# Kernel optimization log

Measured on AMD Instinct MI355X. Metric: run time of the kernel, lower is better.

The kernel has to match this reference:

```python
import jax, jax.numpy as jnp
import numpy as np

V, E, H, L = 32000, 512, 512, 2   # vocab, emb_dim, hidden_dim, lstm layers
IN = 2 * H                        # input_size (= enc_output feature dim)
B, S_ENC, T_DEC = 32, 128, 64


def setup_inputs() -> dict:
    key = jax.random.key(0)
    ks = jax.random.split(key, 20)
    sc = 0.05
    inp = {
        "tokens": jax.random.randint(ks[0], (B, T_DEC), 0, V),
        "enc_output": jax.random.normal(ks[1], (B, S_ENC, IN), jnp.float32),
        "enc_h": jax.random.normal(ks[2], (L, B, H), jnp.float32),
        "enc_c": jax.random.normal(ks[3], (L, B, H), jnp.float32),
        "emb": jax.random.normal(ks[4], (V, E), jnp.float32) * sc,
        # attention MLP: attn1 in = H*L + IN, out = 4H; attn2: 4H -> 1
        "attn1_w": jax.random.normal(ks[5], (4 * H, H * L + IN), jnp.float32) * sc,
        "attn1_b": jnp.zeros((4 * H,), jnp.float32),
        "attn2_w": jax.random.normal(ks[6], (1, 4 * H), jnp.float32) * sc,
        "attn2_b": jnp.zeros((1,), jnp.float32),
        # LSTM layer 0: input E + IN; layer 1: input H. PyTorch gate order i,f,g,o
        "w_ih0": jax.random.normal(ks[7], (4 * H, E + IN), jnp.float32) * sc,
        "w_hh0": jax.random.normal(ks[8], (4 * H, H), jnp.float32) * sc,
        "b_ih0": jnp.zeros((4 * H,), jnp.float32),
        "b_hh0": jnp.zeros((4 * H,), jnp.float32),
        "w_ih1": jax.random.normal(ks[9], (4 * H, H), jnp.float32) * sc,
        "w_hh1": jax.random.normal(ks[10], (4 * H, H), jnp.float32) * sc,
        "b_ih1": jnp.zeros((4 * H,), jnp.float32),
        "b_hh1": jnp.zeros((4 * H,), jnp.float32),
        "out_w": jax.random.normal(ks[11], (V, H), jnp.float32) * sc,
        "out_b": jnp.zeros((V,), jnp.float32),
    }
    return inp


def _lstm_cell(x, h, c, w_ih, w_hh, b_ih, b_hh):
    g = x @ w_ih.T + h @ w_hh.T + (b_ih + b_hh)
    i, f, gg, o = jnp.split(g, 4, axis=-1)
    c_new = jax.nn.sigmoid(f) * c + jax.nn.sigmoid(i) * jnp.tanh(gg)
    h_new = jax.nn.sigmoid(o) * jnp.tanh(c_new)
    return h_new, c_new


def reference(tokens, enc_output, enc_h, enc_c, emb,
              attn1_w, attn1_b, attn2_w, attn2_b,
              w_ih0, w_hh0, b_ih0, b_hh0,
              w_ih1, w_hh1, b_ih1, b_hh1,
              out_w, out_b):
    b, s_enc = enc_output.shape[0], enc_output.shape[1]

    def context(h):  # h: [L, B, H] -> context: [B, 2H]
        hflat = jnp.transpose(h, (1, 0, 2)).reshape(b, -1)          # [B, L*H]
        hexp = jnp.broadcast_to(hflat[:, None, :], (b, s_enc, hflat.shape[-1]))
        ai = jnp.concatenate([enc_output, hexp], axis=-1)           # [B, S, 2H+L*H]
        hid = ai @ attn1_w.T + attn1_b                               # [B, S, 4H]
        logits = hid @ attn2_w.T + attn2_b                           # [B, S, 1]
        w = jax.nn.softmax(logits, axis=1)
        return jnp.sum(enc_output * w, axis=1)                       # [B, 2H]

    def step(carry, emb_t):  # emb_t: [B, E]
        h, c = carry
        ctx = context(h)
        x = jnp.concatenate([emb_t, ctx], axis=-1)                   # [B, E+2H]
        h0, c0 = _lstm_cell(x, h[0], c[0], w_ih0, w_hh0, b_ih0, b_hh0)
        h1, c1 = _lstm_cell(h0, h[1], c[1], w_ih1, w_hh1, b_ih1, b_hh1)
        return (jnp.stack([h0, h1]), jnp.stack([c0, c1])), h1

    emb_seq = jnp.transpose(emb[tokens], (1, 0, 2))                  # [T, B, E]
    _, outs = jax.lax.scan(step, (enc_h, enc_c), emb_seq)            # [T, B, H]
    dec = jnp.transpose(outs, (1, 0, 2))                             # [B, T, H]
    return dec @ out_w.T + out_b                                     # [B, T, V]
```

## Files before the change

### kernel.cpp

```cpp
#include <hip/hip_runtime.h>
#include <hip/hip_bf16.h>

typedef __attribute__((ext_vector_type(4))) float f4v;
typedef __attribute__((ext_vector_type(4))) short s4v;
typedef __attribute__((ext_vector_type(8))) short s8v;

#define DEVINL __device__ __forceinline__
#define NBLK 128
#define PADK 536
#define WROWS (16 * PADK)
#define HSLOT 16384

DEVINL short f2bf(float f) {
  unsigned u = __float_as_uint(f);
  u += 0x7FFFu + ((u >> 16) & 1u);
  return (short)(u >> 16);
}
DEVINL float bf2f(short s) {
  return __uint_as_float(((unsigned)(unsigned short)s) << 16);
}
DEVINL float sigm(float x) { return 1.f / (1.f + expf(-x)); }

DEVINL void cstore64(short* p, unsigned long long d) {
  asm volatile("global_store_dwordx2 %0, %1, off sc0 sc1"
               :: "v"(p), "v"(d) : "memory");
}

__global__ __launch_bounds__(256) void k_init2(const float* __restrict__ enc_h,
                                               short* __restrict__ hbuf,
                                               unsigned* __restrict__ arr) {
  int i = blockIdx.x * 256 + threadIdx.x;
  hbuf[i] = f2bf(enc_h[i]);
  hbuf[(long)65 * HSLOT + i] = f2bf(enc_h[16384 + i]);
  if (i < NBLK * 32 + 32) arr[i] = 0u;
}

__global__ __launch_bounds__(256) void k_weff(const float* __restrict__ attn1_w,
                                              const float* __restrict__ attn2_w,
                                              float* __restrict__ w_enc) {
  __shared__ float part[8][32];
  int t = threadIdx.x;
  int jl = t & 31, kp = t >> 5;
  int j = blockIdx.x * 32 + jl;
  float acc = 0.f;
  for (int k = kp * 256; k < kp * 256 + 256; ++k)
    acc += attn2_w[k] * attn1_w[(long)k * 2048 + j];
  part[kp][jl] = acc;
  __syncthreads();
  if (t < 32) {
    float s = 0.f;
    for (int p = 0; p < 8; ++p) s += part[p][t];
    w_enc[blockIdx.x * 32 + t] = s;
  }
}

__global__ __launch_bounds__(256) void k_attn(const float* __restrict__ enc,
                                              const float* __restrict__ w_enc,
                                              float* __restrict__ ctx) {
  __shared__ float red[256];
  __shared__ float wls[128];
  int b = blockIdx.x, t = threadIdx.x;
  int s = t >> 1, half = t & 1;
  const float* e = enc + ((long)b * 128 + s) * 1024 + half * 512;
  const float* wv = w_enc + half * 512;
  float acc = 0.f;
  for (int k = 0; k < 512; k += 4) {
    f4v ev = *(const f4v*)(e + k);
    f4v w4 = *(const f4v*)(wv + k);
    acc += ev[0] * w4[0] + ev[1] * w4[1] + ev[2] * w4[2] + ev[3] * w4[3];
  }
  red[t] = acc;
  __syncthreads();
  if (half == 0) wls[s] = red[t] + red[t + 1];
  __syncthreads();
  red[t] = (t < 128) ? wls[t] : -3.4e38f;
  __syncthreads();
  for (int off = 128; off >= 1; off >>= 1) {
    if (t < off) red[t] = fmaxf(red[t], red[t + off]);
    __syncthreads();
  }
  float mx = red[0];
  __syncthreads();
  if (t < 128) { float ex = expf(wls[t] - mx); wls[t] = ex; red[t] = ex; }
  else red[t] = 0.f;
  __syncthreads();
  for (int off = 128; off >= 1; off >>= 1) {
    if (t < off) red[t] += red[t + off];
    __syncthreads();
  }
  float inv = 1.f / red[0];
  __syncthreads();
  if (t < 128) wls[t] *= inv;
  __syncthreads();
  float a0 = 0.f, a1 = 0.f, a2 = 0.f, a3 = 0.f;
  for (int ss = 0; ss < 128; ++ss) {
    float w = wls[ss];
    const float* er = enc + ((long)b * 128 + ss) * 1024;
    a0 += w * er[t];
    a1 += w * er[t + 256];
    a2 += w * er[t + 512];
    a3 += w * er[t + 768];
  }
  ctx[b * 1024 + t] = a0;
  ctx[b * 1024 + t + 256] = a1;
  ctx[b * 1024 + t + 512] = a2;
  ctx[b * 1024 + t + 768] = a3;
}

__global__ __launch_bounds__(256) void k_ctxpre(const float* __restrict__ w_ih0,
                                                const float* __restrict__ b_ih0,
                                                const float* __restrict__ b_hh0,
                                                const float* __restrict__ ctx,
                                                float* __restrict__ ctxpre) {
  int t = threadIdx.x;
  int j = blockIdx.x * 8 + (t >> 5);
  int b = t & 31;
  float acc = b_ih0[j] + b_hh0[j];
  const float* w = w_ih0 + (long)j * 1536 + 512;
  const float* c = ctx + b * 1024;
  for (int k = 0; k < 1024; k += 4) {
    f4v wv = *(const f4v*)(w + k);
    f4v cv = *(const f4v*)(c + k);
    acc += wv[0] * cv[0] + wv[1] * cv[1] + wv[2] * cv[2] + wv[3] * cv[3];
  }
  ctxpre[b * 2048 + j] = acc;
}

__global__ __launch_bounds__(256) void k_cvt(const float* __restrict__ src,
                                             short* __restrict__ dst) {
  long i = ((long)blockIdx.x * 256 + threadIdx.x) * 8;
  f4v a = *(const f4v*)(src + i);
  f4v b = *(const f4v*)(src + i + 4);
  s8v o;
  o[0] = f2bf(a[0]); o[1] = f2bf(a[1]); o[2] = f2bf(a[2]); o[3] = f2bf(a[3]);
  o[4] = f2bf(b[0]); o[5] = f2bf(b[1]); o[6] = f2bf(b[2]); o[7] = f2bf(b[3]);
  *(s8v*)(dst + i) = o;
}

template <int MODE>
__global__ __launch_bounds__(256) void gemm_bf16(
    const float* __restrict__ A, const float* __restrict__ B,
    const int* __restrict__ a_rows, const float* __restrict__ bias,
    float* __restrict__ C, int K, int lda, int ldb, int ldc) {
  __shared__ short As[128 * 72];
  __shared__ short Bs[128 * 72];
  int n0 = blockIdx.x * 128, m0 = blockIdx.y * 128;
  int t = threadIdx.x;
  int lane = t & 63, w = t >> 6;
  int wm = w & 1, wn = w >> 1;
  f4v acc[4][4];
#pragma unroll
  for (int mi = 0; mi < 4; ++mi)
#pragma unroll
    for (int ni = 0; ni < 4; ++ni) acc[mi][ni] = (f4v){0.f, 0.f, 0.f, 0.f};

  int sr = t >> 1;
  int sh = (t & 1) * 32;
  long arow = a_rows ? (long)a_rows[m0 + sr] : (long)(m0 + sr);
  const float* ap = A + arow * lda + sh;
  const float* bp = B + (long)(n0 + sr) * ldb + sh;
  short* as = &As[sr * 72 + sh];
  short* bs = &Bs[sr * 72 + sh];

  for (int k0 = 0; k0 < K; k0 += 64) {
#pragma unroll
    for (int i = 0; i < 8; ++i) {
      f4v va = *(const f4v*)(ap + k0 + i * 4);
      f4v vb = *(const f4v*)(bp + k0 + i * 4);
      s4v sa, sb;
      sa[0] = f2bf(va[0]); sa[1] = f2bf(va[1]); sa[2] = f2bf(va[2]); sa[3] = f2bf(va[3]);
      sb[0] = f2bf(vb[0]); sb[1] = f2bf(vb[1]); sb[2] = f2bf(vb[2]); sb[3] = f2bf(vb[3]);
      *(s4v*)(as + i * 4) = sa;
      *(s4v*)(bs + i * 4) = sb;
    }
    __syncthreads();
#pragma unroll
    for (int ks = 0; ks < 2; ++ks) {
      s8v af[4], bf[4];
#pragma unroll
      for (int mi = 0; mi < 4; ++mi)
        af[mi] = *(const s8v*)&As[(wm * 64 + mi * 16 + (lane & 15)) * 72 + ks * 32 + (lane >> 4) * 8];
#pragma unroll
      for (int ni = 0; ni < 4; ++ni)
        bf[ni] = *(const s8v*)&Bs[(wn * 64 + ni * 16 + (lane & 15)) * 72 + ks * 32 + (lane >> 4) * 8];
#pragma unroll
      for (int mi = 0; mi < 4; ++mi)
#pragma unroll
        for (int ni = 0; ni < 4; ++ni)
          acc[mi][ni] = __builtin_amdgcn_mfma_f32_16x16x32_bf16(af[mi], bf[ni], acc[mi][ni], 0, 0, 0);
    }
    __syncthreads();
  }
  int fq = lane >> 4, fr = lane & 15;
#pragma unroll
  for (int mi = 0; mi < 4; ++mi)
#pragma unroll
    for (int ni = 0; ni < 4; ++ni) {
      int col = n0 + wn * 64 + ni * 16 + fr;
      long rowb = m0 + wm * 64 + mi * 16 + fq * 4;
      if (MODE == 2) {
        int bz = (col & 511) >> 2;
        int c = ((col >> 9) << 2) + (col & 3);
#pragma unroll
        for (int r = 0; r < 4; ++r) {
          long m = rowb + r;
          C[(long)bz * 32768 + (m & 63) * 512 + (m >> 6) * 16 + c] = acc[mi][ni][r];
        }
      } else {
        float bv = bias ? bias[col] : 0.f;
#pragma unroll
        for (int r = 0; r < 4; ++r) C[(rowb + r) * (long)ldc + col] = acc[mi][ni][r] + bv;
      }
    }
}

template <bool BCVT>
__global__ __launch_bounds__(256) void gemm_out(
    const short* __restrict__ A, const short* __restrict__ Bbf,
    const float* __restrict__ Bf, const float* __restrict__ bias,
    float* __restrict__ C) {
  __shared__ short As[128 * 72];
  __shared__ short Bs[128 * 72];
  int m0 = blockIdx.x * 128, n0 = blockIdx.y * 128;
  int t = threadIdx.x;
  int lane = t & 63, w = t >> 6;
  int wm = w & 1, wn = w >> 1;
  f4v acc[4][4];
#pragma unroll
  for (int mi = 0; mi < 4; ++mi)
#pragma unroll
    for (int ni = 0; ni < 4; ++ni) acc[mi][ni] = (f4v){0.f, 0.f, 0.f, 0.f};

  int sr = t >> 1;
  int sh = (t & 1) * 32;
  const short* ap = A + (long)(m0 + sr) * 512 + sh;
  const short* bpb = Bbf + (long)(n0 + sr) * 512 + sh;
  const float* bpf = Bf + (long)(n0 + sr) * 512 + sh;
  short* as = &As[sr * 72 + sh];
  short* bs = &Bs[sr * 72 + sh];

  for (int k0 = 0; k0 < 512; k0 += 64) {
#pragma unroll
    for (int i = 0; i < 4; ++i)
      *(s8v*)(as + i * 8) = *(const s8v*)(ap + k0 + i * 8);
    if (BCVT) {
#pragma unroll
      for (int i = 0; i < 8; ++i) {
        f4v vb = *(const f4v*)(bpf + k0 + i * 4);
        s4v sb;
        sb[0] = f2bf(vb[0]); sb[1] = f2bf(vb[1]); sb[2] = f2bf(vb[2]); sb[3] = f2bf(vb[3]);
        *(s4v*)(bs + i * 4) = sb;
      }
    } else {
#pragma unroll
      for (int i = 0; i < 4; ++i)
        *(s8v*)(bs + i * 8) = *(const s8v*)(bpb + k0 + i * 8);
    }
    __syncthreads();
#pragma unroll
    for (int ks = 0; ks < 2; ++ks) {
      s8v af[4], bf[4];
#pragma unroll
      for (int mi = 0; mi < 4; ++mi)
        af[mi] = *(const s8v*)&As[(wm * 64 + mi * 16 + (lane & 15)) * 72 + ks * 32 + (lane >> 4) * 8];
#pragma unroll
      for (int ni = 0; ni < 4; ++ni)
        bf[ni] = *(const s8v*)&Bs[(wn * 64 + ni * 16 + (lane & 15)) * 72 + ks * 32 + (lane >> 4) * 8];
#pragma unroll
      for (int mi = 0; mi < 4; ++mi)
#pragma unroll
        for (int ni = 0; ni < 4; ++ni)
          acc[mi][ni] = __builtin_amdgcn_mfma_f32_16x16x32_bf16(af[mi], bf[ni], acc[mi][ni], 0, 0, 0);
    }
    __syncthreads();
  }
  int fq = lane >> 4, fr = lane & 15;
#pragma unroll
  for (int mi = 0; mi < 4; ++mi)
#pragma unroll
    for (int ni = 0; ni < 4; ++ni) {
      int col = n0 + wn * 64 + ni * 16 + fr;
      float bv = bias[col];
      long rowb = m0 + wm * 64 + mi * 16 + fq * 4;
#pragma unroll
      for (int r = 0; r < 4; ++r)
        __builtin_nontemporal_store(acc[mi][ni][r] + bv, &C[(rowb + r) * 32000L + col]);
    }
}

__global__ __launch_bounds__(256, 1) void lstm_persist(
    const float* __restrict__ w_hh0, const float* __restrict__ w_ih1,
    const float* __restrict__ w_hh1,
    const float* __restrict__ b_ih1, const float* __restrict__ b_hh1,
    const float* __restrict__ enc_c,
    const float* __restrict__ embp2, const float* __restrict__ ctxpre,
    short* __restrict__ hbuf, short* __restrict__ h1seqbf,
    unsigned* __restrict__ arr) {
  __shared__ alignas(16) short wlds[6 * WROWS];
  __shared__ float ctxp_l[32][16];
  __shared__ float bias1_l[16];
  __shared__ float gbuf[2][2][32][17];

  const int tid = threadIdx.x;
  const int hb4 = blockIdx.x * 4;
  const int lane = tid & 63, wid = tid >> 6;
  const int mt = wid & 1, kh = wid >> 1;
  const int fr = lane & 15, fq = lane >> 4;

  for (int base = tid * 4; base < 48 * 512; base += 1024) {
    int row = base >> 9, k = base & 511;
    int m = row >> 4, c = row & 15;
    int j = ((c >> 2) << 9) + hb4 + (c & 3);
    const float* wsrc = (m == 0) ? w_hh0 : ((m == 1) ? w_ih1 : w_hh1);
    f4v v = *(const f4v*)(wsrc + (long)j * 512 + k);
    short* hi = &wlds[(m * 2) * WROWS + c * PADK + k];
    short* lo = &wlds[(m * 2 + 1) * WROWS + c * PADK + k];
#pragma unroll
    for (int e = 0; e < 4; ++e) {
      short hh = f2bf(v[e]);
      hi[e] = hh;
      lo[e] = f2bf(v[e] - bf2f(hh));
    }
  }
  for (int i = tid; i < 512; i += 256) {
    int b = i >> 4, c = i & 15;
    ctxp_l[b][c] = ctxpre[b * 2048 + ((c >> 2) << 9) + hb4 + (c & 3)];
  }
  if (tid < 16) {
    int j = ((tid >> 2) << 9) + hb4 + (tid & 3);
    bias1_l[tid] = b_ih1[j] + b_hh1[j];
  }
  const int cq = (tid & 127) >> 2, cr = tid & 3;
  float c0r = 0.f, c1r = 0.f;
  if (tid < 128) c0r = enc_c[cq * 512 + hb4 + cr];
  else           c1r = enc_c[16384 + cq * 512 + hb4 + cr];
  __syncthreads();
  asm volatile("s_waitcnt vmcnt(0)" ::: "memory");
  asm volatile("buffer_inv sc1" ::: "memory");
  __syncthreads();

  short* H0 = hbuf;
  short* H1 = hbuf + (long)65 * HSLOT;
  const int foff = (mt * 16 + fr) * 512 + kh * 256 + fq * 8;
  const int woff = fr * PADK + kh * 256 + fq * 8;

  for (int p = 0; p <= 64; ++p) {
    const bool do_l0 = (p < 64), do_l1 = (p > 0);
    if (p) {
      if (tid < NBLK)
        while (__hip_atomic_load(&arr[tid << 5], __ATOMIC_RELAXED,
                                 __HIP_MEMORY_SCOPE_AGENT) < (unsigned)p)
          __builtin_amdgcn_s_sleep(2);
      __syncthreads();
    }
    float e4[4] = {0.f, 0.f, 0.f, 0.f};
    if (do_l0 && tid < 128) {
      const float* ep = embp2 + (long)blockIdx.x * 32768 + p * 512 + cq * 16 + cr;
#pragma unroll
      for (int g = 0; g < 4; ++g) e4[g] = ep[g * 4];
    }
    {
      f4v l0h = {0.f, 0.f, 0.f, 0.f}, l0l = l0h;
      f4v x1h = l0h, x1l = l0h, h1h = l0h, h1l = l0h;
      const short* a0 = H0 + (long)p * HSLOT + foff;
      const short* a1 = H1 + (long)(do_l1 ? p - 1 : 0) * HSLOT + foff;
      const short* b0h = &wlds[0 * WROWS + woff];
      const short* b0l = &wlds[1 * WROWS + woff];
      const short* b2h = &wlds[2 * WROWS + woff];
      const short* b2l = &wlds[3 * WROWS + woff];
      const short* b4h = &wlds[4 * WROWS + woff];
      const short* b4l = &wlds[5 * WROWS + woff];
#pragma unroll
      for (int ks = 0; ks < 8; ++ks) {
        s8v A0 = *(const s8v*)(a0 + ks * 32);
        if (do_l0) {
          s8v B0h = *(const s8v*)(b0h + ks * 32);
          s8v B0l = *(const s8v*)(b0l + ks * 32);
          l0h = __builtin_amdgcn_mfma_f32_16x16x32_bf16(A0, B0h, l0h, 0, 0, 0);
          l0l = __builtin_amdgcn_mfma_f32_16x16x32_bf16(A0, B0l, l0l, 0, 0, 0);
        }
        if (do_l1) {
          s8v B2h = *(const s8v*)(b2h + ks * 32);
          s8v B2l = *(const s8v*)(b2l + ks * 32);
          x1h = __builtin_amdgcn_mfma_f32_16x16x32_bf16(A0, B2h, x1h, 0, 0, 0);
          x1l = __builtin_amdgcn_mfma_f32_16x16x32_bf16(A0, B2l, x1l, 0, 0, 0);
          s8v A1 = *(const s8v*)(a1 + ks * 32);
          s8v B4h = *(const s8v*)(b4h + ks * 32);
          s8v B4l = *(const s8v*)(b4l + ks * 32);
          h1h = __builtin_amdgcn_mfma_f32_16x16x32_bf16(A1, B4h, h1h, 0, 0, 0);
          h1l = __builtin_amdgcn_mfma_f32_16x16x32_bf16(A1, B4l, h1l, 0, 0, 0);
        }
      }
      if (do_l0) {
        f4v s = l0h + l0l;
#pragma unroll
        for (int r = 0; r < 4; ++r) gbuf[0][kh][mt * 16 + fq * 4 + r][fr] = s[r];
      }
      if (do_l1) {
        f4v s = x1h + x1l + h1h + h1l;
#pragma unroll
        for (int r = 0; r < 4; ++r) gbuf[1][kh][mt * 16 + fq * 4 + r][fr] = s[r];
      }
    }
    __syncthreads();
    if (tid < 128) {
      if (do_l0) {
        float g4[4];
#pragma unroll
        for (int g = 0; g < 4; ++g) {
          int c = g * 4 + cr;
          g4[g] = gbuf[0][0][cq][c] + gbuf[0][1][cq][c] + ctxp_l[cq][c] + e4[g];
        }
        float cn = sigm(g4[1]) * c0r + sigm(g4[0]) * tanhf(g4[2]);
        float hn = sigm(g4[3]) * tanhf(cn);
        c0r = cn;
        unsigned v16 = (unsigned)(unsigned short)f2bf(hn);
        unsigned p01 = v16 | ((unsigned)__shfl_down((int)v16, 1) << 16);
        unsigned long long wd = (unsigned long long)p01 |
            ((unsigned long long)(unsigned)__shfl_down((int)p01, 2) << 32);
        if ((tid & 3) == 0)
          cstore64(H0 + (long)(p + 1) * HSLOT + cq * 512 + hb4, wd);
      }
    } else if (do_l1) {
      float g4[4];
#pragma unroll
      for (int g = 0; g < 4; ++g) {
        int c = g * 4 + cr;
        g4[g] = gbuf[1][0][cq][c] + gbuf[1][1][cq][c] + bias1_l[c];
      }
      float cn = sigm(g4[1]) * c1r + sigm(g4[0]) * tanhf(g4[2]);
      float hn = sigm(g4[3]) * tanhf(cn);
      c1r = cn;
      unsigned v16 = (unsigned)(unsigned short)f2bf(hn);
      unsigned p01 = v16 | ((unsigned)__shfl_down((int)v16, 1) << 16);
      unsigned long long wd = (unsigned long long)p01 |
          ((unsigned long long)(unsigned)__shfl_down((int)p01, 2) << 32);
      if ((tid & 3) == 0) {
        if (p < 64)
          cstore64(H1 + (long)p * HSLOT + cq * 512 + hb4, wd);
        *(unsigned long long*)&h1seqbf[((long)cq * 64 + (p - 1)) * 512 + hb4] = wd;
      }
    }
    if (p < 64) {
      asm volatile("s_waitcnt vmcnt(0)" ::: "memory");
      __syncthreads();
      if (tid == 0)
        __hip_atomic_store(&arr[(unsigned)blockIdx.x << 5], (unsigned)(p + 1),
                           __ATOMIC_RELAXED, __HIP_MEMORY_SCOPE_AGENT);
    }
  }
}

extern "C" void kernel_launch(void* const* d_in, const int* in_sizes, int n_in,
                              void* d_out, int out_size, void* d_ws, size_t ws_size,
                              hipStream_t stream) {
  const int*   tokens  = (const int*)  d_in[0];
  const float* enc_out = (const float*)d_in[1];
  const float* enc_h   = (const float*)d_in[2];
  const float* enc_c   = (const float*)d_in[3];
  const float* emb     = (const float*)d_in[4];
  const float* attn1_w = (const float*)d_in[5];
  const float* attn2_w = (const float*)d_in[7];
  const float* w_ih0   = (const float*)d_in[9];
  const float* w_hh0   = (const float*)d_in[10];
  const float* b_ih0   = (const float*)d_in[11];
  const float* b_hh0   = (const float*)d_in[12];
  const float* w_ih1   = (const float*)d_in[13];
  const float* w_hh1   = (const float*)d_in[14];
  const float* b_ih1   = (const float*)d_in[15];
  const float* b_hh1   = (const float*)d_in[16];
  const float* out_w   = (const float*)d_in[17];
  const float* out_b   = (const float*)d_in[18];
  float* out = (float*)d_out;

  float* f = (float*)d_ws;
  float*    w_enc    = f;
  float*    ctx      = f + 1024;
  float*    ctxpre   = f + 33792;
  float*    embp2    = f + 99328;
  short*    h1seqbf  = (short*)(f + 4293632);
  short*    hbuf     = (short*)(f + 4817920);
  unsigned* arr      = (unsigned*)(f + 5882880);
  short*    out_w_bf = (short*)(f + 5887040);
  const size_t NEED = (size_t)(5887040 + 8192000) * 4;
  const bool big = ws_size >= NEED;

  k_init2<<<64, 256, 0, stream>>>(enc_h, hbuf, arr);
  k_weff<<<32, 256, 0, stream>>>(attn1_w, attn2_w, w_enc);
  k_attn<<<32, 256, 0, stream>>>(enc_out, w_enc, ctx);
  k_ctxpre<<<256, 256, 0, stream>>>(w_ih0, b_ih0, b_hh0, ctx, ctxpre);
  gemm_bf16<2><<<dim3(16, 16), 256, 0, stream>>>(emb, w_ih0, tokens, nullptr,
                                                 embp2, 512, 512, 1536, 0);
  if (big) k_cvt<<<8000, 256, 0, stream>>>(out_w, out_w_bf);
  lstm_persist<<<NBLK, 256, 0, stream>>>(w_hh0, w_ih1, w_hh1, b_ih1, b_hh1, enc_c,
                                         embp2, ctxpre, hbuf, h1seqbf, arr);
  if (big)
    gemm_out<false><<<dim3(16, 250), 256, 0, stream>>>(h1seqbf, out_w_bf, nullptr,
                                                       out_b, out);
  else
    gemm_out<true><<<dim3(16, 250), 256, 0, stream>>>(h1seqbf, nullptr, out_w,
                                                      out_b, out);
}
```

Baseline: 635.6 us.

## Split per-step barrier into separate layer-0 and layer-1 flags to overlap layers

Each block now publishes separate arrival flags for layer 0 and layer 1 (layer-1 flag initialized to 1). Layer 0's h update is signalled right after its cell update, so other blocks can proceed before the layer-1 work finishes. Layer 1 computes its input projection from h0 first, then waits only on the layer-1 flag before reading h1. The embedding prefetch is moved ahead of the spin-wait and the sleep interval is shortened. This shortens the critical path of the recurrent grid barrier, at the cost of an extra spin-wait and more syncthreads per step.

```diff
diff --git a/kernel.cpp b/kernel.cpp
--- a/kernel.cpp
+++ b/kernel.cpp
@@ -32,7 +32,7 @@
   int i = blockIdx.x * 256 + threadIdx.x;
   hbuf[i] = f2bf(enc_h[i]);
   hbuf[(long)65 * HSLOT + i] = f2bf(enc_h[16384 + i]);
-  if (i < NBLK * 32 + 32) arr[i] = 0u;
+  if (i < NBLK * 32 + 32) arr[i] = ((i & 31) == 16) ? 1u : 0u;
 }
 
 __global__ __launch_bounds__(256) void k_weff(const float* __restrict__ attn1_w,
@@ -346,65 +346,41 @@
 
   for (int p = 0; p <= 64; ++p) {
     const bool do_l0 = (p < 64), do_l1 = (p > 0);
+    float e4[4] = {0.f, 0.f, 0.f, 0.f};
+    if (do_l0 && tid < 128) {
+      const float* ep = embp2 + (long)blockIdx.x * 32768 + p * 512 + cq * 16 + cr;
+#pragma unroll
+      for (int g = 0; g < 4; ++g) e4[g] = ep[g * 4];
+    }
     if (p) {
       if (tid < NBLK)
         while (__hip_atomic_load(&arr[tid << 5], __ATOMIC_RELAXED,
                                  __HIP_MEMORY_SCOPE_AGENT) < (unsigned)p)
-          __builtin_amdgcn_s_sleep(2);
+          __builtin_amdgcn_s_sleep(1);
       __syncthreads();
     }
-    float e4[4] = {0.f, 0.f, 0.f, 0.f};
-    if (do_l0 && tid < 128) {
-      const float* ep = embp2 + (long)blockIdx.x * 32768 + p * 512 + cq * 16 + cr;
-#pragma unroll
-      for (int g = 0; g < 4; ++g) e4[g] = ep[g * 4];
-    }
-    {
+    const short* a0 = H0 + (long)p * HSLOT + foff;
+    s8v A0[8];
+#pragma unroll
+    for (int ks = 0; ks < 8; ++ks) A0[ks] = *(const s8v*)(a0 + ks * 32);
+    if (do_l0) {
       f4v l0h = {0.f, 0.f, 0.f, 0.f}, l0l = l0h;
-      f4v x1h = l0h, x1l = l0h, h1h = l0h, h1l = l0h;
-      const short* a0 = H0 + (long)p * HSLOT + foff;
-      const short* a1 = H1 + (long)(do_l1 ? p - 1 : 0) * HSLOT + foff;
       const short* b0h = &wlds[0 * WROWS + woff];
       const short* b0l = &wlds[1 * WROWS + woff];
-      const short* b2h = &wlds[2 * WROWS + woff];
-      const short* b2l = &wlds[3 * WROWS + woff];
-      const short* b4h = &wlds[4 * WROWS + woff];
-      const short* b4l = &wlds[5 * WROWS + woff];
 #pragma unroll
       for (int ks = 0; ks < 8; ++ks) {
-        s8v A0 = *(const s8v*)(a0 + ks * 32);
-        if (do_l0) {
-          s8v B0h = *(const s8v*)(b0h + ks * 32);
-          s8v B0l = *(const s8v*)(b0l + ks * 32);
-          l0h = __builtin_amdgcn_mfma_f32_16x16x32_bf16(A0, B0h, l0h, 0, 0, 0);
-          l0l = __builtin_amdgcn_mfma_f32_16x16x32_bf16(A0, B0l, l0l, 0, 0, 0);
-        }
-        if (do_l1) {
-          s8v B2h = *(const s8v*)(b2h + ks * 32);
-          s8v B2l = *(const s8v*)(b2l + ks * 32);
-          x1h = __builtin_amdgcn_mfma_f32_16x16x32_bf16(A0, B2h, x1h, 0, 0, 0);
-          x1l = __builtin_amdgcn_mfma_f32_16x16x32_bf16(A0, B2l, x1l, 0, 0, 0);
-          s8v A1 = *(const s8v*)(a1 + ks * 32);
-          s8v B4h = *(const s8v*)(b4h + ks * 32);
-          s8v B4l = *(const s8v*)(b4l + ks * 32);
-          h1h = __builtin_amdgcn_mfma_f32_16x16x32_bf16(A1, B4h, h1h, 0, 0, 0);
-          h1l = __builtin_amdgcn_mfma_f32_16x16x32_bf16(A1, B4l, h1l, 0, 0, 0);
-        }
-      }
-      if (do_l0) {
-        f4v s = l0h + l0l;
-#pragma unroll
-        for (int r = 0; r < 4; ++r) gbuf[0][kh][mt * 16 + fq * 4 + r][fr] = s[r];
-      }
-      if (do_l1) {
-        f4v s = x1h + x1l + h1h + h1l;
-#pragma unroll
-        for (int r = 0; r < 4; ++r) gbuf[1][kh][mt * 16 + fq * 4 + r][fr] = s[r];
-      }
-    }
-    __syncthreads();
-    if (tid < 128) {
-      if (do_l0) {
+        s8v B0h = *(const s8v*)(b0h + ks * 32);
+        s8v B0l = *(const s8v*)(b0l + ks * 32);
+        l0h = __builtin_amdgcn_mfma_f32_16x16x32_bf16(A0[ks], B0h, l0h, 0, 0, 0);
+        l0l = __builtin_amdgcn_mfma_f32_16x16x32_bf16(A0[ks], B0l, l0l, 0, 0, 0);
+      }
+      f4v s = l0h + l0l;
+#pragma unroll
+      for (int r = 0; r < 4; ++r) gbuf[0][kh][mt * 16 + fq * 4 + r][fr] = s[r];
+    }
+    __syncthreads();
+    if (do_l0) {
+      if (tid < 128) {
         float g4[4];
 #pragma unroll
         for (int g = 0; g < 4; ++g) {
@@ -421,32 +397,71 @@
         if ((tid & 3) == 0)
           cstore64(H0 + (long)(p + 1) * HSLOT + cq * 512 + hb4, wd);
       }
-    } else if (do_l1) {
-      float g4[4];
-#pragma unroll
-      for (int g = 0; g < 4; ++g) {
-        int c = g * 4 + cr;
-        g4[g] = gbuf[1][0][cq][c] + gbuf[1][1][cq][c] + bias1_l[c];
-      }
-      float cn = sigm(g4[1]) * c1r + sigm(g4[0]) * tanhf(g4[2]);
-      float hn = sigm(g4[3]) * tanhf(cn);
-      c1r = cn;
-      unsigned v16 = (unsigned)(unsigned short)f2bf(hn);
-      unsigned p01 = v16 | ((unsigned)__shfl_down((int)v16, 1) << 16);
-      unsigned long long wd = (unsigned long long)p01 |
-          ((unsigned long long)(unsigned)__shfl_down((int)p01, 2) << 32);
-      if ((tid & 3) == 0) {
-        if (p < 64)
-          cstore64(H1 + (long)p * HSLOT + cq * 512 + hb4, wd);
-        *(unsigned long long*)&h1seqbf[((long)cq * 64 + (p - 1)) * 512 + hb4] = wd;
-      }
-    }
-    if (p < 64) {
       asm volatile("s_waitcnt vmcnt(0)" ::: "memory");
       __syncthreads();
       if (tid == 0)
         __hip_atomic_store(&arr[(unsigned)blockIdx.x << 5], (unsigned)(p + 1),
                            __ATOMIC_RELAXED, __HIP_MEMORY_SCOPE_AGENT);
+    }
+    if (do_l1) {
+      f4v x1h = {0.f, 0.f, 0.f, 0.f}, x1l = x1h, h1h = x1h, h1l = x1h;
+      const short* b2h = &wlds[2 * WROWS + woff];
+      const short* b2l = &wlds[3 * WROWS + woff];
+#pragma unroll
+      for (int ks = 0; ks < 8; ++ks) {
+        s8v B2h = *(const s8v*)(b2h + ks * 32);
+        s8v B2l = *(const s8v*)(b2l + ks * 32);
+        x1h = __builtin_amdgcn_mfma_f32_16x16x32_bf16(A0[ks], B2h, x1h, 0, 0, 0);
+        x1l = __builtin_amdgcn_mfma_f32_16x16x32_bf16(A0[ks], B2l, x1l, 0, 0, 0);
+      }
+      if (tid < NBLK)
+        while (__hip_atomic_load(&arr[(tid << 5) + 16], __ATOMIC_RELAXED,
+                                 __HIP_MEMORY_SCOPE_AGENT) < (unsigned)p)
+          __builtin_amdgcn_s_sleep(1);
+      __syncthreads();
+      const short* a1 = H1 + (long)(p - 1) * HSLOT + foff;
+      const short* b4h = &wlds[4 * WROWS + woff];
+      const short* b4l = &wlds[5 * WROWS + woff];
+#pragma unroll
+      for (int ks = 0; ks < 8; ++ks) {
+        s8v A1 = *(const s8v*)(a1 + ks * 32);
+        s8v B4h = *(const s8v*)(b4h + ks * 32);
+        s8v B4l = *(const s8v*)(b4l + ks * 32);
+        h1h = __builtin_amdgcn_mfma_f32_16x16x32_bf16(A1, B4h, h1h, 0, 0, 0);
+        h1l = __builtin_amdgcn_mfma_f32_16x16x32_bf16(A1, B4l, h1l, 0, 0, 0);
+      }
+      f4v s = x1h + x1l + h1h + h1l;
+#pragma unroll
+      for (int r = 0; r < 4; ++r) gbuf[1][kh][mt * 16 + fq * 4 + r][fr] = s[r];
+      __syncthreads();
+      if (tid >= 128) {
+        float g4[4];
+#pragma unroll
+        for (int g = 0; g < 4; ++g) {
+          int c = g * 4 + cr;
+          g4[g] = gbuf[1][0][cq][c] + gbuf[1][1][cq][c] + bias1_l[c];
+        }
+        float cn = sigm(g4[1]) * c1r + sigm(g4[0]) * tanhf(g4[2]);
+        float hn = sigm(g4[3]) * tanhf(cn);
+        c1r = cn;
+        unsigned v16 = (unsigned)(unsigned short)f2bf(hn);
+        unsigned p01 = v16 | ((unsigned)__shfl_down((int)v16, 1) << 16);
+        unsigned long long wd = (unsigned long long)p01 |
+            ((unsigned long long)(unsigned)__shfl_down((int)p01, 2) << 32);
+        if ((tid & 3) == 0) {
+          if (p < 64)
+            cstore64(H1 + (long)p * HSLOT + cq * 512 + hb4, wd);
+          *(unsigned long long*)&h1seqbf[((long)cq * 64 + (p - 1)) * 512 + hb4] = wd;
+        }
+      }
+      if (p < 64) {
+        asm volatile("s_waitcnt vmcnt(0)" ::: "memory");
+        __syncthreads();
+        if (tid == 0)
+          __hip_atomic_store(&arr[((unsigned)blockIdx.x << 5) + 16],
+                             (unsigned)(p + 1), __ATOMIC_RELAXED,
+                             __HIP_MEMORY_SCOPE_AGENT);
+      }
     }
   }
 }
```

Result: no change. 644.9 us (+1.5%).
